# Kernel tuning notes

Measured on AMD Instinct MI355X. Metric: run time of the kernel, lower is better.

The kernel has to match this reference:

```python
import jax, jax.numpy as jnp
import numpy as np

B, S, H = 2, 2048, 256
NS, NR = 512, 512
FFN_RATIO = 4


def setup_inputs() -> dict:
    key = jax.random.key(0)
    ks = jax.random.split(key, 8)
    token_reps = jax.random.normal(ks[0], (B, S, H), dtype=jnp.float32)
    token_masks = jnp.ones((B, S), dtype=bool)
    span_reps = jax.random.normal(ks[1], (B, NS, H), dtype=jnp.float32)
    # spans: start in [0, S-16), length in [1, 16) -> valid [start, end) windows
    starts = jax.random.randint(ks[2], (B, NS), 0, S - 16)
    lens = jax.random.randint(ks[3], (B, NS), 1, 16)
    span_ids = jnp.stack([starts, starts + lens], axis=-1)  # (B, NS, 2)
    rel_ids = jax.random.randint(ks[4], (B, NR, 2), 0, NS)  # (B, NR, 2)
    rel_masks = jnp.ones((B, NR), dtype=bool)
    neg_limit = jnp.float32(-6.0e4)
    d_in = 3 * H
    d_ff = FFN_RATIO * d_in
    W1 = jax.random.normal(ks[5], (d_in, d_ff), dtype=jnp.float32) / np.float32(np.sqrt(d_in))
    b1 = jnp.zeros((d_ff,), dtype=jnp.float32)
    W2 = jax.random.normal(ks[6], (d_ff, H), dtype=jnp.float32) / np.float32(np.sqrt(d_ff))
    b2 = jnp.zeros((H,), dtype=jnp.float32)
    return {
        "token_reps": token_reps, "token_masks": token_masks,
        "span_reps": span_reps, "span_ids": span_ids,
        "rel_ids": rel_ids, "rel_masks": rel_masks, "neg_limit": neg_limit,
        "W1": W1, "b1": b1, "W2": W2, "b2": b2,
    }


def reference(token_reps, token_masks, span_reps, span_ids, rel_ids, rel_masks,
              neg_limit, W1, b1, W2, b2):
    seq_len = token_reps.shape[1]
    head_ids = rel_ids[..., 0]  # (B, NR)
    tail_ids = rel_ids[..., 1]
    # gather head/tail span reps: (B, NR, H)
    head_reps = jnp.take_along_axis(span_reps, head_ids[..., None], axis=1)
    tail_reps = jnp.take_along_axis(span_reps, tail_ids[..., None], axis=1)
    # span boundaries per relation: (B, NR)
    head_start = jnp.take_along_axis(span_ids[..., 0], head_ids, axis=1)
    head_end = jnp.take_along_axis(span_ids[..., 1], head_ids, axis=1)
    tail_start = jnp.take_along_axis(span_ids[..., 0], tail_ids, axis=1)
    tail_end = jnp.take_along_axis(span_ids[..., 1], tail_ids, axis=1)
    seq = jnp.arange(seq_len)[None, None, :]  # (1, 1, S)
    head_m = (seq >= head_start[..., None]) & (seq < head_end[..., None])
    tail_m = (seq >= tail_start[..., None]) & (seq < tail_end[..., None])
    # 'between' base context: tokens strictly between the two spans
    lo = jnp.minimum(head_end, tail_end)[..., None]
    hi = jnp.maximum(head_start, tail_start)[..., None]
    base = (seq >= lo) & (seq < hi)
    ctx_mask = base & ~(head_m | tail_m) & rel_masks[..., None] & token_masks[:, None, :]  # (B, NR, S)
    # masked max-pool over seq: (B, NR, S, H) -> (B, NR, H)
    masked = jnp.where(ctx_mask[..., None], token_reps[:, None, :, :], neg_limit)
    context_reps = jnp.max(masked, axis=2)
    # no-context fallback: fully-masked relations -> zero vector
    all_masked = jnp.all(context_reps == neg_limit, axis=-1)
    context_reps = jnp.where(all_masked[..., None], jnp.float32(0.0), context_reps)
    rel_reps = jnp.concatenate([head_reps, tail_reps, context_reps], axis=-1)  # (B, NR, 3H)
    h = jax.nn.relu(rel_reps @ W1 + b1)  # dropout = identity at inference
    return h @ W2 + b2
```

## Files before the change

kernel.cpp:

```cpp
#include <hip/hip_runtime.h>
#include <hip/hip_bf16.h>
#include <stdint.h>

#define Bb 2
#define Ss 2048
#define Hh 256
#define NSs 512
#define NRr 512
#define DIN 768
#define DFF 3072
#define Mm (Bb*NRr)
#define LVLS 10
#define KSLICES 4

typedef __attribute__((ext_vector_type(8))) short short8;
typedef __attribute__((ext_vector_type(4))) short short4b;
typedef __attribute__((ext_vector_type(4))) float floatx4;
typedef __attribute__((ext_vector_type(2))) float floatx2;

__device__ __forceinline__ short f2bf(float f) {
  uint32_t u = __float_as_uint(f);
  u += 0x7fffu + ((u >> 16) & 1u);
  return (short)(u >> 16);
}

__device__ __forceinline__ short4b f2bf4(floatx4 v) {
  short4b r;
  r.x = f2bf(v.x); r.y = f2bf(v.y); r.z = f2bf(v.z); r.w = f2bf(v.w);
  return r;
}

__device__ __forceinline__ floatx4 max4(floatx4 a, floatx4 b) {
  floatx4 r;
  r.x = fmaxf(a.x, b.x); r.y = fmaxf(a.y, b.y);
  r.z = fmaxf(a.z, b.z); r.w = fmaxf(a.w, b.w);
  return r;
}

__device__ __forceinline__ uint32_t pack_bf2_rne(float lo, float hi) {
  uint32_t ul = __float_as_uint(lo); ul += 0x7fffu + ((ul >> 16) & 1u);
  uint32_t uh = __float_as_uint(hi); uh += 0x7fffu + ((uh >> 16) & 1u);
  return (uh & 0xffff0000u) | (ul >> 16);
}

__device__ __forceinline__ uint32_t max_packed(uint32_t a, uint32_t b) {
  float a0 = __uint_as_float(a << 16), a1 = __uint_as_float(a & 0xffff0000u);
  float b0 = __uint_as_float(b << 16), b1 = __uint_as_float(b & 0xffff0000u);
  float m0 = fmaxf(a0, b0), m1 = fmaxf(a1, b1);
  return (__float_as_uint(m1) & 0xffff0000u) | (__float_as_uint(m0) >> 16);
}

__device__ __forceinline__ void gld_lds16(const void* g, void* l) {
  __builtin_amdgcn_global_load_lds(
      (const __attribute__((address_space(1))) void*)g,
      (__attribute__((address_space(3))) void*)l, 16, 0, 0);
}

__global__ __launch_bounds__(256) void sparse_levels(
    const float* __restrict__ token_reps,
    uint32_t* __restrict__ T)
{
  __shared__ uint32_t lds[Ss];
  int t = threadIdx.x;
  int bid = blockIdx.x;
  int b = bid >> 7;
  int r = bid & 127;
  int L = ((r >> 6) & 1) * 8 + (r & 7);
  int m = (r >> 3) & 7;
  int g = L * 8 + m;
  int c2 = g * 2;

#pragma unroll
  for (int j = 0; j < 8; ++j) {
    int i = j * 256 + t;
    floatx2 v = *(const floatx2*)&token_reps[((size_t)b * Ss + i) * Hh + c2];
    lds[i] = pack_bf2_rne(v.x, v.y);
  }
  __syncthreads();

  for (int k = 1; k <= LVLS; ++k) {
    int d = 1 << (k - 1);
    uint32_t val[8];
#pragma unroll
    for (int j = 0; j < 8; ++j) {
      int i = j * 256 + t;
      val[j] = max_packed(lds[i], lds[min(i + d, Ss - 1)]);
    }
    __syncthreads();
    uint32_t* Tk = T + (((size_t)(k - 1) * Bb + b) * 128 + g) * Ss;
#pragma unroll
    for (int j = 0; j < 8; ++j) {
      int i = j * 256 + t;
      lds[i] = val[j];
      Tk[i] = val[j];
    }
    __syncthreads();
  }
}

__global__ __launch_bounds__(256) void query_and_convT(
    const float* __restrict__ token_reps,
    const float* __restrict__ span_reps,
    const int* __restrict__ span_ids,
    const int* __restrict__ rel_ids,
    const uint32_t* __restrict__ T,
    short* __restrict__ X,
    const float* __restrict__ W1, short* __restrict__ W1t,
    const float* __restrict__ W2, short* __restrict__ W2t)
{
  __shared__ float tile[32][33];
  int bid = blockIdx.x;
  int tid = threadIdx.x;

  if (bid < Mm / 4) {
    int w = tid >> 6, lane = tid & 63;
    int br = bid * 4 + w;
    int b = br >> 9, r = br & (NRr - 1);

    int hid = rel_ids[(b * NRr + r) * 2 + 0];
    int tid_ = rel_ids[(b * NRr + r) * 2 + 1];
    int hs = span_ids[(b * NSs + hid) * 2 + 0];
    int he = span_ids[(b * NSs + hid) * 2 + 1];
    int ts = span_ids[(b * NSs + tid_) * 2 + 0];
    int te = span_ids[(b * NSs + tid_) * 2 + 1];
    int lo = min(he, te);
    int hi = max(hs, ts);

    int s1 = hs, e1 = he, s2 = ts, e2 = te;
    if (s2 < s1) { s1 = ts; e1 = te; s2 = hs; e2 = he; }

    int ia[3], ib[3], ni = 0;
    if (e1 >= s2) {
      int me = max(e1, e2);
      int a = lo, bb = min(hi, s1); if (a < bb) { ia[ni] = a; ib[ni] = bb; ni++; }
      a = max(lo, me); bb = hi;     if (a < bb) { ia[ni] = a; ib[ni] = bb; ni++; }
    } else {
      int a = lo, bb = min(hi, s1);       if (a < bb) { ia[ni] = a; ib[ni] = bb; ni++; }
      a = max(lo, e1); bb = min(hi, s2);  if (a < bb) { ia[ni] = a; ib[ni] = bb; ni++; }
      a = max(lo, e2); bb = hi;           if (a < bb) { ia[ni] = a; ib[ni] = bb; ni++; }
    }

    int c4 = lane * 4;
    floatx4 acc = {-3.4e38f, -3.4e38f, -3.4e38f, -3.4e38f};
    for (int q = 0; q < ni; ++q) {
      int a = ia[q], len = ib[q] - a;
      int k = 31 - __builtin_clz(len);
      if (k == 0) {
        acc = max4(acc, *(const floatx4*)&token_reps[((size_t)b * Ss + a) * Hh + c4]);
      } else {
        const uint32_t* P = T + (((size_t)(k - 1) * Bb + b) * 128 + 2 * lane) * Ss;
        int a2 = ib[q] - (1 << k);
#pragma unroll
        for (int pass = 0; pass < 2; ++pass) {
          int aa = pass ? a2 : a;
          uint32_t u0 = P[aa], u1 = P[Ss + aa];
          floatx4 v;
          v.x = __uint_as_float(u0 << 16); v.y = __uint_as_float(u0 & 0xffff0000u);
          v.z = __uint_as_float(u1 << 16); v.w = __uint_as_float(u1 & 0xffff0000u);
          acc = max4(acc, v);
        }
      }
    }
    floatx4 ctx;
    if (ni > 0) ctx = acc;
    else        ctx = (floatx4){0.f, 0.f, 0.f, 0.f};

    floatx4 hr = *(const floatx4*)&span_reps[((size_t)b * NSs + hid) * Hh + c4];
    floatx4 tr = *(const floatx4*)&span_reps[((size_t)b * NSs + tid_) * Hh + c4];
    size_t base = (size_t)br * DIN;
    *(short4b*)&X[base + c4]          = f2bf4(hr);
    *(short4b*)&X[base + Hh + c4]     = f2bf4(tr);
    *(short4b*)&X[base + 2 * Hh + c4] = f2bf4(ctx);
  } else {
    int cb = bid - Mm / 4;
    const float* W; short* Wt; int K, N, bx, by;
    if (cb < 2304) { W = W1; Wt = W1t; K = DIN; N = DFF; bx = cb % 96; by = cb / 96; }
    else { cb -= 2304; W = W2; Wt = W2t; K = DFF; N = Hh; bx = cb % 8; by = cb / 8; }
    int n0 = bx * 32, k0 = by * 32;
    int tx = tid & 31, ty = tid >> 5;
#pragma unroll
    for (int i = 0; i < 4; ++i)
      tile[ty + i * 8][tx] = W[(size_t)(k0 + ty + i * 8) * N + n0 + tx];
    __syncthreads();
#pragma unroll
    for (int i = 0; i < 4; ++i)
      Wt[(size_t)(n0 + ty + i * 8) * K + k0 + tx] = f2bf(tile[tx][ty + i * 8]);
  }
}

__global__ __launch_bounds__(256) void ctx_kernel(
    const float* __restrict__ token_reps,
    const float* __restrict__ span_reps,
    const int* __restrict__ span_ids,
    const int* __restrict__ rel_ids,
    short* __restrict__ X)
{
  int br = blockIdx.x;
  int b = br >> 9;
  int r = br & (NRr - 1);
  int c = threadIdx.x;

  int hid = rel_ids[(b * NRr + r) * 2 + 0];
  int tid = rel_ids[(b * NRr + r) * 2 + 1];
  int hs = span_ids[(b * NSs + hid) * 2 + 0];
  int he = span_ids[(b * NSs + hid) * 2 + 1];
  int ts = span_ids[(b * NSs + tid) * 2 + 0];
  int te = span_ids[(b * NSs + tid) * 2 + 1];
  int lo = min(he, te);
  int hi = max(hs, ts);

  float m = -3.4e38f;
  bool found = false;
  const float* tr = token_reps + ((size_t)b * Ss) * Hh + c;
  for (int s = lo; s < hi; ++s) {
    bool inspan = (s >= hs && s < he) || (s >= ts && s < te);
    if (!inspan) { found = true; m = fmaxf(m, tr[(size_t)s * Hh]); }
  }
  float ctx = found ? m : 0.0f;

  size_t base = (size_t)br * DIN;
  X[base + c]          = f2bf(span_reps[((size_t)b * NSs + hid) * Hh + c]);
  X[base + Hh + c]     = f2bf(span_reps[((size_t)b * NSs + tid) * Hh + c]);
  X[base + 2 * Hh + c] = f2bf(ctx);
}

__global__ void convT(const float* __restrict__ W, short* __restrict__ Wt,
                      int K, int N) {
  __shared__ float tile[32][33];
  int n0 = blockIdx.x * 32, k0 = blockIdx.y * 32;
  int tx = threadIdx.x, ty = threadIdx.y;
#pragma unroll
  for (int i = 0; i < 4; ++i)
    tile[ty + i * 8][tx] = W[(size_t)(k0 + ty + i * 8) * N + n0 + tx];
  __syncthreads();
#pragma unroll
  for (int i = 0; i < 4; ++i)
    Wt[(size_t)(n0 + ty + i * 8) * K + k0 + tx] = f2bf(tile[tx][ty + i * 8]);
}

template <int BM, int BN, bool RELU_BF16>
__global__ __launch_bounds__(256) void gemm_bt(
    const short* __restrict__ A, const short* __restrict__ Bt,
    const float* __restrict__ bias, void* __restrict__ Cout,
    int M, int N, int K) {
  constexpr int BK = 32;
  constexpr int WM = BM / 2, WN = BN / 2;
  constexpr int MT = WM / 16, NT = WN / 16;
  __shared__ __align__(16) short As[BM * BK];
  __shared__ __align__(16) short Bs[BN * BK];

  int tid = threadIdx.x;
  int lane = tid & 63, w = tid >> 6;
  int wi = w & 1, wj = w >> 1;
  int m0 = blockIdx.x * BM, n0 = blockIdx.y * BN;
  int quad = lane >> 4, l16 = lane & 15;

  floatx4 acc[MT][NT];
#pragma unroll
  for (int i = 0; i < MT; ++i)
#pragma unroll
    for (int j = 0; j < NT; ++j)
      acc[i][j] = (floatx4){0.f, 0.f, 0.f, 0.f};

  constexpr int ACH = BM / 16;
  constexpr int BCH = BN / 16;

  for (int kk = 0; kk < K; kk += BK) {
#pragma unroll
    for (int i = 0; i < ACH / 4; ++i) {
      int chunk = w * (ACH / 4) + i;
      int r = chunk * 16 + (lane >> 2);
      gld_lds16(A + (size_t)(m0 + r) * K + kk + (lane & 3) * 8, &As[chunk * 512]);
    }
#pragma unroll
    for (int i = 0; i < BCH / 4; ++i) {
      int chunk = w * (BCH / 4) + i;
      int r = chunk * 16 + (lane >> 2);
      gld_lds16(Bt + (size_t)(n0 + r) * K + kk + (lane & 3) * 8, &Bs[chunk * 512]);
    }
    __syncthreads();

    short8 a[MT], b[NT];
#pragma unroll
    for (int i = 0; i < MT; ++i)
      a[i] = *(const short8*)&As[(wi * WM + i * 16 + l16) * BK + quad * 8];
#pragma unroll
    for (int j = 0; j < NT; ++j)
      b[j] = *(const short8*)&Bs[(wj * WN + j * 16 + l16) * BK + quad * 8];
#pragma unroll
    for (int i = 0; i < MT; ++i)
#pragma unroll
      for (int j = 0; j < NT; ++j)
        acc[i][j] = __builtin_amdgcn_mfma_f32_16x16x32_bf16(a[i], b[j],
                                                            acc[i][j], 0, 0, 0);
    __syncthreads();
  }

#pragma unroll
  for (int i = 0; i < MT; ++i) {
#pragma unroll
    for (int j = 0; j < NT; ++j) {
      int col = n0 + wj * WN + j * 16 + l16;
      float bv = bias[col];
#pragma unroll
      for (int rr = 0; rr < 4; ++rr) {
        int row = m0 + wi * WM + i * 16 + quad * 4 + rr;
        float v = acc[i][j][rr] + bv;
        if (RELU_BF16) {
          v = fmaxf(v, 0.f);
          ((short*)Cout)[(size_t)row * N + col] = f2bf(v);
        } else {
          ((float*)Cout)[(size_t)row * N + col] = v;
        }
      }
    }
  }
}

__global__ __launch_bounds__(256) void gemm_bt_splitk(
    const short* __restrict__ A, const short* __restrict__ Bt,
    float* __restrict__ P, int M, int N, int K) {
  constexpr int BM = 64, BN = 64, BK = 32;
  constexpr int WM = 32, WN = 32;
  constexpr int MT = 2, NT = 2;
  __shared__ __align__(16) short As[BM * BK];
  __shared__ __align__(16) short Bs[BN * BK];

  int tid = threadIdx.x;
  int lane = tid & 63, w = tid >> 6;
  int wi = w & 1, wj = w >> 1;
  int m0 = blockIdx.x * BM, n0 = blockIdx.y * BN;
  int z = blockIdx.z;
  int ksl = K / KSLICES;
  int k_begin = z * ksl, k_end = k_begin + ksl;
  int quad = lane >> 4, l16 = lane & 15;

  floatx4 acc[MT][NT];
#pragma unroll
  for (int i = 0; i < MT; ++i)
#pragma unroll
    for (int j = 0; j < NT; ++j)
      acc[i][j] = (floatx4){0.f, 0.f, 0.f, 0.f};

  for (int kk = k_begin; kk < k_end; kk += BK) {
    {
      int r = w * 16 + (lane >> 2);
      gld_lds16(A + (size_t)(m0 + r) * K + kk + (lane & 3) * 8, &As[w * 512]);
      int rb = w * 16 + (lane >> 2);
      gld_lds16(Bt + (size_t)(n0 + rb) * K + kk + (lane & 3) * 8, &Bs[w * 512]);
    }
    __syncthreads();

    short8 a[MT], b[NT];
#pragma unroll
    for (int i = 0; i < MT; ++i)
      a[i] = *(const short8*)&As[(wi * WM + i * 16 + l16) * BK + quad * 8];
#pragma unroll
    for (int j = 0; j < NT; ++j)
      b[j] = *(const short8*)&Bs[(wj * WN + j * 16 + l16) * BK + quad * 8];
#pragma unroll
    for (int i = 0; i < MT; ++i)
#pragma unroll
      for (int j = 0; j < NT; ++j)
        acc[i][j] = __builtin_amdgcn_mfma_f32_16x16x32_bf16(a[i], b[j],
                                                            acc[i][j], 0, 0, 0);
    __syncthreads();
  }

  float* Pz = P + (size_t)z * M * N;
#pragma unroll
  for (int i = 0; i < MT; ++i)
#pragma unroll
    for (int j = 0; j < NT; ++j) {
      int col = n0 + wj * WN + j * 16 + l16;
#pragma unroll
      for (int rr = 0; rr < 4; ++rr) {
        int row = m0 + wi * WM + i * 16 + quad * 4 + rr;
        Pz[(size_t)row * N + col] = acc[i][j][rr];
      }
    }
}

__global__ __launch_bounds__(256) void splitk_reduce(
    const float* __restrict__ P, const float* __restrict__ bias,
    float* __restrict__ out) {
  int idx = (blockIdx.x * 256 + threadIdx.x) * 4;
  int col = idx & (Hh - 1);
  floatx4 s = *(const floatx4*)&bias[col];
#pragma unroll
  for (int z = 0; z < KSLICES; ++z)
    s += *(const floatx4*)&P[(size_t)z * Mm * Hh + idx];
  *(floatx4*)&out[idx] = s;
}

extern "C" void kernel_launch(void* const* d_in, const int* in_sizes, int n_in,
                              void* d_out, int out_size, void* d_ws,
                              size_t ws_size, hipStream_t stream) {
  const float*   token_reps  = (const float*)d_in[0];
  const float*   span_reps   = (const float*)d_in[2];
  const int*     span_ids    = (const int*)d_in[3];
  const int*     rel_ids     = (const int*)d_in[4];
  const float*   W1 = (const float*)d_in[7];
  const float*   b1 = (const float*)d_in[8];
  const float*   W2 = (const float*)d_in[9];
  const float*   b2 = (const float*)d_in[10];
  float* out = (float*)d_out;

  char* ws = (char*)d_ws;
  short* X    = (short*)ws;
  short* W1t  = X + (size_t)Mm * DIN;
  short* W2t  = W1t + (size_t)DFF * DIN;
  short* hbuf = W2t + (size_t)Hh * DFF;
  size_t bf16_elems = (size_t)Mm * DIN + (size_t)DFF * DIN +
                      (size_t)Hh * DFF + (size_t)Mm * DFF;
  size_t off = (bf16_elems * sizeof(short) + 255) & ~(size_t)255;
  float* Pbuf = (float*)(ws + off);
  off += (size_t)KSLICES * Mm * Hh * sizeof(float);
  off = (off + 255) & ~(size_t)255;
  uint32_t* T = (uint32_t*)(ws + off);
  size_t need = off + (size_t)LVLS * Bb * 128 * Ss * sizeof(uint32_t);

  bool fast = (ws_size >= need);
  if (fast) {
    hipLaunchKernelGGL(sparse_levels, dim3(256), dim3(256), 0, stream,
                       token_reps, T);
    hipLaunchKernelGGL(query_and_convT, dim3(Mm / 4 + 2304 + 768), dim3(256),
                       0, stream, token_reps, span_reps, span_ids, rel_ids, T,
                       X, W1, W1t, W2, W2t);
  } else {
    hipLaunchKernelGGL(ctx_kernel, dim3(Mm), dim3(256), 0, stream,
                       token_reps, span_reps, span_ids, rel_ids, X);
    hipLaunchKernelGGL(convT, dim3(DFF / 32, DIN / 32), dim3(32, 8), 0, stream,
                       W1, W1t, DIN, DFF);
    hipLaunchKernelGGL(convT, dim3(Hh / 32, DFF / 32), dim3(32, 8), 0, stream,
                       W2, W2t, DFF, Hh);
  }
  hipLaunchKernelGGL((gemm_bt<64, 128, true>), dim3(Mm / 64, DFF / 128),
                     dim3(256), 0, stream, X, W1t, b1, (void*)hbuf, Mm, DFF, DIN);
  if (fast) {
    hipLaunchKernelGGL(gemm_bt_splitk, dim3(Mm / 64, Hh / 64, KSLICES),
                       dim3(256), 0, stream, hbuf, W2t, Pbuf, Mm, Hh, DFF);
    hipLaunchKernelGGL(splitk_reduce, dim3(Mm * Hh / 1024), dim3(256), 0,
                       stream, Pbuf, b2, out);
  } else {
    hipLaunchKernelGGL((gemm_bt<64, 64, false>), dim3(Mm / 64, Hh / 64),
                       dim3(256), 0, stream, hbuf, W2t, b2, (void*)out,
                       Mm, Hh, DFF);
  }
}
```

Before: 128.6 us.

## Keep sparse-table levels in LDS and answer context queries in-block

The sparse max table is no longer written to global memory across 10 levels. Each block builds 8 levels (up to width 128) in 64KB of LDS for its channel pair and then answers all 512 relation queries for that batch directly. Ranges of 128 or more are covered by stepping through level-7 windows. This removes roughly 40MB of global table writes and the scattered global reads in the query kernel. In exchange, each thread may loop over long ranges, and the heavy LDS use limits occupancy.

```diff
diff --git a/kernel.cpp b/kernel.cpp
--- a/kernel.cpp
+++ b/kernel.cpp
@@ -10,7 +10,6 @@
 #define DIN 768
 #define DFF 3072
 #define Mm (Bb*NRr)
-#define LVLS 10
 #define KSLICES 4
 
 typedef __attribute__((ext_vector_type(8))) short short8;
@@ -27,13 +26,6 @@
 __device__ __forceinline__ short4b f2bf4(floatx4 v) {
   short4b r;
   r.x = f2bf(v.x); r.y = f2bf(v.y); r.z = f2bf(v.z); r.w = f2bf(v.w);
-  return r;
-}
-
-__device__ __forceinline__ floatx4 max4(floatx4 a, floatx4 b) {
-  floatx4 r;
-  r.x = fmaxf(a.x, b.x); r.y = fmaxf(a.y, b.y);
-  r.z = fmaxf(a.z, b.z); r.w = fmaxf(a.w, b.w);
   return r;
 }
 
@@ -56,17 +48,19 @@
       (__attribute__((address_space(3))) void*)l, 16, 0, 0);
 }
 
-__global__ __launch_bounds__(256) void sparse_levels(
+__global__ __launch_bounds__(256) void ctx_lds(
     const float* __restrict__ token_reps,
-    uint32_t* __restrict__ T)
+    const int* __restrict__ span_ids,
+    const int* __restrict__ rel_ids,
+    short* __restrict__ X)
 {
-  __shared__ uint32_t lds[Ss];
+  __shared__ uint32_t Lv[8][Ss];
   int t = threadIdx.x;
   int bid = blockIdx.x;
   int b = bid >> 7;
-  int r = bid & 127;
-  int L = ((r >> 6) & 1) * 8 + (r & 7);
-  int m = (r >> 3) & 7;
+  int r7 = bid & 127;
+  int L = ((r7 >> 6) & 1) * 8 + (r7 & 7);
+  int m = (r7 >> 3) & 7;
   int g = L * 8 + m;
   int c2 = g * 2;
 
@@ -74,36 +68,65 @@
   for (int j = 0; j < 8; ++j) {
     int i = j * 256 + t;
     floatx2 v = *(const floatx2*)&token_reps[((size_t)b * Ss + i) * Hh + c2];
-    lds[i] = pack_bf2_rne(v.x, v.y);
+    Lv[0][i] = pack_bf2_rne(v.x, v.y);
   }
   __syncthreads();
-
-  for (int k = 1; k <= LVLS; ++k) {
+#pragma unroll
+  for (int k = 1; k <= 7; ++k) {
     int d = 1 << (k - 1);
-    uint32_t val[8];
 #pragma unroll
     for (int j = 0; j < 8; ++j) {
       int i = j * 256 + t;
-      val[j] = max_packed(lds[i], lds[min(i + d, Ss - 1)]);
-    }
-    __syncthreads();
-    uint32_t* Tk = T + (((size_t)(k - 1) * Bb + b) * 128 + g) * Ss;
-#pragma unroll
-    for (int j = 0; j < 8; ++j) {
-      int i = j * 256 + t;
-      lds[i] = val[j];
-      Tk[i] = val[j];
-    }
-    __syncthreads();
-  }
-}
-
-__global__ __launch_bounds__(256) void query_and_convT(
-    const float* __restrict__ token_reps,
+      Lv[k][i] = max_packed(Lv[k - 1][i], Lv[k - 1][min(i + d, Ss - 1)]);
+    }
+    __syncthreads();
+  }
+
+#pragma unroll
+  for (int rr = 0; rr < 2; ++rr) {
+    int r = rr * 256 + t;
+    int hid = rel_ids[(b * NRr + r) * 2 + 0];
+    int tid_ = rel_ids[(b * NRr + r) * 2 + 1];
+    int hs = span_ids[(b * NSs + hid) * 2 + 0];
+    int he = span_ids[(b * NSs + hid) * 2 + 1];
+    int ts = span_ids[(b * NSs + tid_) * 2 + 0];
+    int te = span_ids[(b * NSs + tid_) * 2 + 1];
+    int lo = min(he, te), hi = max(hs, ts);
+    int s1 = hs, e1 = he, s2 = ts, e2 = te;
+    if (s2 < s1) { s1 = ts; e1 = te; s2 = hs; e2 = he; }
+
+    int ia[3], ibv[3], ni = 0;
+    if (e1 >= s2) {
+      int me = max(e1, e2);
+      int a = lo, bb2 = min(hi, s1); if (a < bb2) { ia[ni]=a; ibv[ni]=bb2; ni++; }
+      a = max(lo, me); bb2 = hi;     if (a < bb2) { ia[ni]=a; ibv[ni]=bb2; ni++; }
+    } else {
+      int a = lo, bb2 = min(hi, s1);      if (a < bb2) { ia[ni]=a; ibv[ni]=bb2; ni++; }
+      a = max(lo, e1); bb2 = min(hi, s2); if (a < bb2) { ia[ni]=a; ibv[ni]=bb2; ni++; }
+      a = max(lo, e2); bb2 = hi;          if (a < bb2) { ia[ni]=a; ibv[ni]=bb2; ni++; }
+    }
+
+    uint32_t acc = 0xff80ff80u;
+    for (int q = 0; q < ni; ++q) {
+      int a = ia[q], e = ibv[q], len = e - a;
+      if (len >= 128) {
+        int x = a;
+        for (; x + 128 <= e; x += 128) acc = max_packed(acc, Lv[7][x]);
+        if (x < e) acc = max_packed(acc, Lv[7][e - 128]);
+      } else {
+        int k = 31 - __builtin_clz(len);
+        acc = max_packed(acc, Lv[k][a]);
+        acc = max_packed(acc, Lv[k][e - (1 << k)]);
+      }
+    }
+    if (ni == 0) acc = 0;
+    *(uint32_t*)&X[(size_t)(b * NRr + r) * DIN + 2 * Hh + c2] = acc;
+  }
+}
+
+__global__ __launch_bounds__(256) void gather_and_convT(
     const float* __restrict__ span_reps,
-    const int* __restrict__ span_ids,
     const int* __restrict__ rel_ids,
-    const uint32_t* __restrict__ T,
     short* __restrict__ X,
     const float* __restrict__ W1, short* __restrict__ W1t,
     const float* __restrict__ W2, short* __restrict__ W2t)
@@ -116,61 +139,14 @@
     int w = tid >> 6, lane = tid & 63;
     int br = bid * 4 + w;
     int b = br >> 9, r = br & (NRr - 1);
-
     int hid = rel_ids[(b * NRr + r) * 2 + 0];
     int tid_ = rel_ids[(b * NRr + r) * 2 + 1];
-    int hs = span_ids[(b * NSs + hid) * 2 + 0];
-    int he = span_ids[(b * NSs + hid) * 2 + 1];
-    int ts = span_ids[(b * NSs + tid_) * 2 + 0];
-    int te = span_ids[(b * NSs + tid_) * 2 + 1];
-    int lo = min(he, te);
-    int hi = max(hs, ts);
-
-    int s1 = hs, e1 = he, s2 = ts, e2 = te;
-    if (s2 < s1) { s1 = ts; e1 = te; s2 = hs; e2 = he; }
-
-    int ia[3], ib[3], ni = 0;
-    if (e1 >= s2) {
-      int me = max(e1, e2);
-      int a = lo, bb = min(hi, s1); if (a < bb) { ia[ni] = a; ib[ni] = bb; ni++; }
-      a = max(lo, me); bb = hi;     if (a < bb) { ia[ni] = a; ib[ni] = bb; ni++; }
-    } else {
-      int a = lo, bb = min(hi, s1);       if (a < bb) { ia[ni] = a; ib[ni] = bb; ni++; }
-      a = max(lo, e1); bb = min(hi, s2);  if (a < bb) { ia[ni] = a; ib[ni] = bb; ni++; }
-      a = max(lo, e2); bb = hi;           if (a < bb) { ia[ni] = a; ib[ni] = bb; ni++; }
-    }
-
     int c4 = lane * 4;
-    floatx4 acc = {-3.4e38f, -3.4e38f, -3.4e38f, -3.4e38f};
-    for (int q = 0; q < ni; ++q) {
-      int a = ia[q], len = ib[q] - a;
-      int k = 31 - __builtin_clz(len);
-      if (k == 0) {
-        acc = max4(acc, *(const floatx4*)&token_reps[((size_t)b * Ss + a) * Hh + c4]);
-      } else {
-        const uint32_t* P = T + (((size_t)(k - 1) * Bb + b) * 128 + 2 * lane) * Ss;
-        int a2 = ib[q] - (1 << k);
-#pragma unroll
-        for (int pass = 0; pass < 2; ++pass) {
-          int aa = pass ? a2 : a;
-          uint32_t u0 = P[aa], u1 = P[Ss + aa];
-          floatx4 v;
-          v.x = __uint_as_float(u0 << 16); v.y = __uint_as_float(u0 & 0xffff0000u);
-          v.z = __uint_as_float(u1 << 16); v.w = __uint_as_float(u1 & 0xffff0000u);
-          acc = max4(acc, v);
-        }
-      }
-    }
-    floatx4 ctx;
-    if (ni > 0) ctx = acc;
-    else        ctx = (floatx4){0.f, 0.f, 0.f, 0.f};
-
     floatx4 hr = *(const floatx4*)&span_reps[((size_t)b * NSs + hid) * Hh + c4];
     floatx4 tr = *(const floatx4*)&span_reps[((size_t)b * NSs + tid_) * Hh + c4];
     size_t base = (size_t)br * DIN;
-    *(short4b*)&X[base + c4]          = f2bf4(hr);
-    *(short4b*)&X[base + Hh + c4]     = f2bf4(tr);
-    *(short4b*)&X[base + 2 * Hh + c4] = f2bf4(ctx);
+    *(short4b*)&X[base + c4]      = f2bf4(hr);
+    *(short4b*)&X[base + Hh + c4] = f2bf4(tr);
   } else {
     int cb = bid - Mm / 4;
     const float* W; short* Wt; int K, N, bx, by;
@@ -199,7 +175,6 @@
   int b = br >> 9;
   int r = br & (NRr - 1);
   int c = threadIdx.x;
-
   int hid = rel_ids[(b * NRr + r) * 2 + 0];
   int tid = rel_ids[(b * NRr + r) * 2 + 1];
   int hs = span_ids[(b * NSs + hid) * 2 + 0];
@@ -208,7 +183,6 @@
   int te = span_ids[(b * NSs + tid) * 2 + 1];
   int lo = min(he, te);
   int hi = max(hs, ts);
-
   float m = -3.4e38f;
   bool found = false;
   const float* tr = token_reps + ((size_t)b * Ss) * Hh + c;
@@ -217,7 +191,6 @@
     if (!inspan) { found = true; m = fmaxf(m, tr[(size_t)s * Hh]); }
   }
   float ctx = found ? m : 0.0f;
-
   size_t base = (size_t)br * DIN;
   X[base + c]          = f2bf(span_reps[((size_t)b * NSs + hid) * Hh + c]);
   X[base + Hh + c]     = f2bf(span_reps[((size_t)b * NSs + tid) * Hh + c]);
@@ -346,8 +319,7 @@
     {
       int r = w * 16 + (lane >> 2);
       gld_lds16(A + (size_t)(m0 + r) * K + kk + (lane & 3) * 8, &As[w * 512]);
-      int rb = w * 16 + (lane >> 2);
-      gld_lds16(Bt + (size_t)(n0 + rb) * K + kk + (lane & 3) * 8, &Bs[w * 512]);
+      gld_lds16(Bt + (size_t)(n0 + r) * K + kk + (lane & 3) * 8, &Bs[w * 512]);
     }
     __syncthreads();
 
@@ -415,18 +387,14 @@
                       (size_t)Hh * DFF + (size_t)Mm * DFF;
   size_t off = (bf16_elems * sizeof(short) + 255) & ~(size_t)255;
   float* Pbuf = (float*)(ws + off);
-  off += (size_t)KSLICES * Mm * Hh * sizeof(float);
-  off = (off + 255) & ~(size_t)255;
-  uint32_t* T = (uint32_t*)(ws + off);
-  size_t need = off + (size_t)LVLS * Bb * 128 * Ss * sizeof(uint32_t);
+  size_t need = off + (size_t)KSLICES * Mm * Hh * sizeof(float);
 
   bool fast = (ws_size >= need);
   if (fast) {
-    hipLaunchKernelGGL(sparse_levels, dim3(256), dim3(256), 0, stream,
-                       token_reps, T);
-    hipLaunchKernelGGL(query_and_convT, dim3(Mm / 4 + 2304 + 768), dim3(256),
-                       0, stream, token_reps, span_reps, span_ids, rel_ids, T,
-                       X, W1, W1t, W2, W2t);
+    hipLaunchKernelGGL(ctx_lds, dim3(256), dim3(256), 0, stream,
+                       token_reps, span_ids, rel_ids, X);
+    hipLaunchKernelGGL(gather_and_convT, dim3(Mm / 4 + 2304 + 768), dim3(256),
+                       0, stream, span_reps, rel_ids, X, W1, W1t, W2, W2t);
   } else {
     hipLaunchKernelGGL(ctx_kernel, dim3(Mm), dim3(256), 0, stream,
                        token_reps, span_reps, span_ids, rel_ids, X);
```

Result: faster. 123.1 us (-4.3%).
